# Kernel optimization log

Measured on AMD Instinct MI355X. Metric: run time of the kernel, lower is better.

## Reference

```python
import jax, jax.numpy as jnp
import numpy as np

MAX_CONTEXT = 100
NUM_HEADS = 4
GRU_GROUPS = 4


def _layernorm(x, g, b, eps=1e-5):
    m = jnp.mean(x, axis=-1, keepdims=True)
    v = jnp.mean((x - m) ** 2, axis=-1, keepdims=True)
    return (x - m) / jnp.sqrt(v + eps) * g + b


def _grouped_gru(x, wih, whh, bih, bhh, G):
    # x: [N, T, C]; shared GRU params run on each channel group (PyTorch gate order r,z,n)
    N, T, C = x.shape
    D = C // G
    xg = x.reshape(N, T, G, D)
    xp = jnp.einsum('ntgd,ed->ntge', xg, wih) + bih  # e = 3D, precomputed input projections
    xp = jnp.moveaxis(xp, 1, 0)  # [T, N, G, 3D]

    def step(h, xt):
        gh = jnp.einsum('ngd,ed->nge', h, whh) + bhh
        xr, xz, xn = jnp.split(xt, 3, axis=-1)
        hr, hz, hn = jnp.split(gh, 3, axis=-1)
        r = jax.nn.sigmoid(xr + hr)
        z = jax.nn.sigmoid(xz + hz)
        n = jnp.tanh(xn + r * hn)
        h = (1.0 - z) * n + z * h
        return h, h

    h0 = jnp.zeros((N, G, D), x.dtype)
    _, hs = jax.lax.scan(step, h0, xp)  # hs: [T, N, G, D]
    return jnp.moveaxis(hs, 0, 1).reshape(N, T, C)


def _mha(x, wqkv, bqkv, wo, bo, H, max_ctx):
    # batch_first self-attention with causal + truncated-window additive mask
    N, T, C = x.shape
    Dh = C // H
    qkv = x @ wqkv.T + bqkv
    q, k, v = jnp.split(qkv, 3, axis=-1)
    q = q.reshape(N, T, H, Dh)
    k = k.reshape(N, T, H, Dh)
    v = v.reshape(N, T, H, Dh)
    scale = 1.0 / np.sqrt(Dh).astype(np.float32)
    scores = jnp.einsum('nqhd,nkhd->nhqk', q, k) * scale
    i = jnp.arange(T)
    diff = i[:, None] - i[None, :]
    allowed = (diff >= 0) & (diff <= max_ctx)
    scores = jnp.where(allowed, scores, -jnp.inf)
    attn = jax.nn.softmax(scores, axis=-1)
    out = jnp.einsum('nhqk,nkhd->nqhd', attn, v).reshape(N, T, C)
    return out @ wo.T + bo


def setup_inputs() -> dict:
    key = jax.random.key(0)
    ks = jax.random.split(key, 5)
    B, C, T, F = 2, 128, 512, 64
    D = C // GRU_GROUPS
    s = 0.1
    return {
        'x': jax.random.normal(ks[0], (B, C, T, F), jnp.float32),
        'ln1_g': jnp.ones((C,), jnp.float32),
        'ln1_b': jnp.zeros((C,), jnp.float32),
        'gru_wih': jax.random.normal(ks[1], (3 * D, D), jnp.float32) * s,
        'gru_whh': jax.random.normal(ks[2], (3 * D, D), jnp.float32) * s,
        'gru_bih': jnp.zeros((3 * D,), jnp.float32),
        'gru_bhh': jnp.zeros((3 * D,), jnp.float32),
        'ln2_g': jnp.ones((C,), jnp.float32),
        'ln2_b': jnp.zeros((C,), jnp.float32),
        'in_proj_w': jax.random.normal(ks[3], (3 * C, C), jnp.float32) * s,
        'in_proj_b': jnp.zeros((3 * C,), jnp.float32),
        'out_proj_w': jax.random.normal(ks[4], (C, C), jnp.float32) * s,
        'out_proj_b': jnp.zeros((C,), jnp.float32),
    }


def reference(x, ln1_g, ln1_b, gru_wih, gru_whh, gru_bih, gru_bhh, ln2_g, ln2_b, in_proj_w, in_proj_b, out_proj_w, out_proj_b):
    B, C, T, F = x.shape
    # [B, C, T, F] -> [B*F, T, C]: each freq bin is an independent time sequence
    seq = jnp.transpose(x, (0, 3, 2, 1)).reshape(B * F, T, C)
    seq = seq + _grouped_gru(_layernorm(seq, ln1_g, ln1_b), gru_wih, gru_whh, gru_bih, gru_bhh, GRU_GROUPS)
    seq = seq + _mha(_layernorm(seq, ln2_g, ln2_b), in_proj_w, in_proj_b, out_proj_w, out_proj_b, NUM_HEADS, MAX_CONTEXT)
    return jnp.transpose(seq.reshape(B, F, T, C), (0, 3, 2, 1))
```

## Files before the change

### kernel.cpp

```cpp
#include <hip/hip_runtime.h>
#include <hip/hip_bf16.h>
#include <math.h>


typedef __attribute__((ext_vector_type(8))) short short8;
typedef __attribute__((ext_vector_type(4))) float f32x4;
typedef __attribute__((ext_vector_type(2))) float f32x2;

__device__ __forceinline__ float bflo(unsigned int u) { return __uint_as_float(u << 16); }
__device__ __forceinline__ float bfhi(unsigned int u) { return __uint_as_float(u & 0xffff0000u); }
__device__ __forceinline__ float bf2f(unsigned short u) { return __uint_as_float(((unsigned int)u) << 16); }
__device__ __forceinline__ unsigned short f2bf(float f) {
  __hip_bfloat16 h = __float2bfloat16(f);
  return *reinterpret_cast<unsigned short*>(&h);
}

typedef __attribute__((address_space(1))) const unsigned int uint_g;
typedef __attribute__((address_space(3))) unsigned int uint_l;
__device__ __forceinline__ void glds16(const void* g, void* l) {
  __builtin_amdgcn_global_load_lds((uint_g*)g, (uint_l*)l, 16, 0, 0);
}

__global__ void cvt_all_kernel(const float* __restrict__ a, unsigned short* __restrict__ da,
                               const float* __restrict__ b, unsigned short* __restrict__ db,
                               const float* __restrict__ c, unsigned short* __restrict__ dc) {
  int i = blockIdx.x * 256 + threadIdx.x;
  if (i < 3072) da[i] = f2bf(a[i]);
  else if (i < 3072 + 49152) db[i - 3072] = f2bf(b[i - 3072]);
  else if (i < 3072 + 49152 + 16384) dc[i - 52224] = f2bf(c[i - 52224]);
}

__global__ __launch_bounds__(256) void transpose_in_ln_kernel(const float* __restrict__ x,
                                                              float* __restrict__ seq,
                                                              const float* __restrict__ gam,
                                                              const float* __restrict__ bet,
                                                              unsigned short* __restrict__ out) {
  __shared__ float tile[128 * 65];
  int b = blockIdx.x >> 9;
  int t = blockIdx.x & 511;
  for (int i = threadIdx.x; i < 128 * 64; i += 256) {
    int c = i >> 6, f = i & 63;
    tile[c * 65 + f] = x[(((size_t)(b * 128 + c)) * 512 + t) * 64 + f];
  }
  __syncthreads();
  for (int i = threadIdx.x; i < 64 * 128; i += 256) {
    int f = i >> 7, c = i & 127;
    seq[(((size_t)(b * 64 + f)) * 512 + t) * 128 + c] = tile[c * 65 + f];
  }

  const int f = threadIdx.x >> 2, q = threadIdx.x & 3;
  float s = 0.f, ss = 0.f;
  #pragma unroll
  for (int u = 0; u < 32; ++u) {
    float v = tile[(q * 32 + u) * 65 + f];
    s += v; ss += v * v;
  }
  s += __shfl_xor(s, 1); s += __shfl_xor(s, 2);
  ss += __shfl_xor(ss, 1); ss += __shfl_xor(ss, 2);
  float mean = s * (1.f / 128.f);
  float var = ss * (1.f / 128.f) - mean * mean;
  float rs = rsqrtf(var + 1e-5f);

  unsigned int* orow = (unsigned int*)(out + (((size_t)(b * 64 + f)) * 512 + t) * 128);
  #pragma unroll
  for (int u = 0; u < 8; ++u) {
    int c0 = q * 32 + u * 4;
    float4 gg = ((const float4*)gam)[c0 >> 2];
    float4 bb = ((const float4*)bet)[c0 >> 2];
    float v0 = tile[(c0 + 0) * 65 + f], v1 = tile[(c0 + 1) * 65 + f];
    float v2 = tile[(c0 + 2) * 65 + f], v3 = tile[(c0 + 3) * 65 + f];
    float o0 = (v0 - mean) * rs * gg.x + bb.x;
    float o1 = (v1 - mean) * rs * gg.y + bb.y;
    float o2 = (v2 - mean) * rs * gg.z + bb.z;
    float o3 = (v3 - mean) * rs * gg.w + bb.w;
    orow[(c0 >> 1) + 0] = ((unsigned int)f2bf(o1) << 16) | (unsigned int)f2bf(o0);
    orow[(c0 >> 1) + 1] = ((unsigned int)f2bf(o3) << 16) | (unsigned int)f2bf(o2);
  }
}

__global__ __launch_bounds__(256) void transpose_out_kernel(const float* __restrict__ seq, float* __restrict__ out) {
  __shared__ float tile[128 * 65];
  int b = blockIdx.x >> 9;
  int t = blockIdx.x & 511;
  for (int i = threadIdx.x; i < 64 * 128; i += 256) {
    int f = i >> 7, c = i & 127;
    tile[c * 65 + f] = seq[(((size_t)(b * 64 + f)) * 512 + t) * 128 + c];
  }
  __syncthreads();
  for (int i = threadIdx.x; i < 128 * 64; i += 256) {
    int c = i >> 6, f = i & 63;
    out[(((size_t)(b * 128 + c)) * 512 + t) * 64 + f] = tile[c * 65 + f];
  }
}

__global__ __launch_bounds__(256) void ln_kernel(const float* __restrict__ in, const float* __restrict__ g,
                                                 const float* __restrict__ b, unsigned short* __restrict__ out) {
  int row = blockIdx.x * 4 + (threadIdx.x >> 6);
  int lane = threadIdx.x & 63;
  float2 v = ((const float2*)(in + (size_t)row * 128))[lane];
  float s = v.x + v.y, ss = v.x * v.x + v.y * v.y;
  #pragma unroll
  for (int off = 32; off > 0; off >>= 1) {
    s += __shfl_xor(s, off);
    ss += __shfl_xor(ss, off);
  }
  float mean = s * (1.f / 128.f);
  float var = ss * (1.f / 128.f) - mean * mean;
  float rs = rsqrtf(var + 1e-5f);
  float2 gg = ((const float2*)g)[lane];
  float2 bb = ((const float2*)b)[lane];
  float o0 = (v.x - mean) * rs * gg.x + bb.x;
  float o1 = (v.y - mean) * rs * gg.y + bb.y;
  unsigned int packed = ((unsigned int)f2bf(o1) << 16) | (unsigned int)f2bf(o0);
  ((unsigned int*)(out + (size_t)row * 128))[lane] = packed;
}

template <int K, int MODE>
__global__ __launch_bounds__(256) void gemm_mfma(const unsigned short* __restrict__ A,
                                                 const unsigned short* __restrict__ W,
                                                 const float* __restrict__ bias,
                                                 unsigned short* __restrict__ outB,
                                                 float* __restrict__ outF, int Ncols) {
  const int tid = threadIdx.x;
  const int wave = tid >> 6, lane = tid & 63;
  const int wy = wave >> 1, wx = wave & 1;
  const int lr = lane & 15, lq = lane >> 4;
  const int m0 = blockIdx.x * 128 + wy * 64;
  const int n0 = blockIdx.y * 128 + wx * 64;

  f32x4 acc[4][4];
  #pragma unroll
  for (int i = 0; i < 4; ++i)
    #pragma unroll
    for (int j = 0; j < 4; ++j) acc[i][j] = f32x4{0.f, 0.f, 0.f, 0.f};

  const short8 zfrag = short8{0, 0, 0, 0, 0, 0, 0, 0};

  #pragma unroll
  for (int kk = 0; kk < K; kk += 32) {
    short8 af[4], bfq[4];
    #pragma unroll
    for (int i = 0; i < 4; ++i)
      af[i] = *(const short8*)(A + (size_t)(m0 + i * 16 + lr) * K + kk + lq * 8);
    #pragma unroll
    for (int j = 0; j < 4; ++j) {
      int wr = n0 + j * 16 + lr;
      bfq[j] = (wr < Ncols) ? *(const short8*)(W + (size_t)wr * K + kk + lq * 8) : zfrag;
    }
    #pragma unroll
    for (int i = 0; i < 4; ++i)
      #pragma unroll
      for (int j = 0; j < 4; ++j)
        acc[i][j] = __builtin_amdgcn_mfma_f32_16x16x32_bf16(af[i], bfq[j], acc[i][j], 0, 0, 0);
  }

  #pragma unroll
  for (int j = 0; j < 4; ++j) {
    int col = n0 + j * 16 + lr;
    if (col < Ncols) {
      float bb = bias[col];
      #pragma unroll
      for (int i = 0; i < 4; ++i) {
        #pragma unroll
        for (int r = 0; r < 4; ++r) {
          int row = m0 + i * 16 + lq * 4 + r;
          float v = acc[i][j][r] + bb;
          if (MODE == 0)
            outB[(size_t)row * Ncols + col] = f2bf(v);
          else
            outF[(size_t)row * 128 + col] += v;
        }
      }
    }
  }
}

__global__ __launch_bounds__(64, 1) void gru_kernel(const unsigned short* __restrict__ xp,
                                                    const float* __restrict__ whh,
                                                    const float* __restrict__ bhh,
                                                    float* __restrict__ seq) {
  const int l = threadIdx.x;
  const int half = l >> 5, d = l & 31;
  const int blk = blockIdx.x;
  const int chain = blk * 2 + half;
  const int n = chain >> 2;
  const int g0 = (blk * 2) & 3;

  const float LOG2E = 1.4426950408889634f;
  const float T2LOG2E = 2.8853900817779268f;

  __shared__ __align__(16) unsigned char stage[2][6144];
  __shared__ __align__(16) float h_lds[2][64];
  h_lds[0][l] = 0.f;

  f32x2 wr2[16], wz2[16], wn2[16];
  #pragma unroll
  for (int u = 0; u < 16; ++u) {
    float2 a = *(const float2*)(whh + (size_t)d * 32 + u * 2);
    float2 b = *(const float2*)(whh + (size_t)(32 + d) * 32 + u * 2);
    float2 c = *(const float2*)(whh + (size_t)(64 + d) * 32 + u * 2);
    wr2[u] = f32x2{a.x * LOG2E, a.y * LOG2E};
    wz2[u] = f32x2{b.x * LOG2E, b.y * LOG2E};
    wn2[u] = f32x2{c.x * T2LOG2E, c.y * T2LOG2E};
  }
  #pragma unroll
  for (int u = 0; u < 16; ++u)
    asm volatile("" : "+v"(wr2[u]), "+v"(wz2[u]), "+v"(wn2[u]));

  float br = bhh[d] * LOG2E, bz = bhh[32 + d] * LOG2E, bn = bhh[64 + d] * T2LOG2E;
  asm volatile("" : "+v"(br), "+v"(bz), "+v"(bn));

  const char* xg = (const char*)xp;
  const size_t cb0 = ((size_t)n * 2048 + g0) * 192;
  const size_t cb1 = ((size_t)n * 2048 + g0 + 1) * 192;
  const int fa = l * 16;
  const int oxa = (fa / 192) * 768 + (fa % 192);
  const int fb = 1024 + l * 16;
  const int oxb = (fb / 192) * 768 + (fb % 192);
  const char* px0a = xg + cb0 + oxa;
  const char* px0b = xg + cb0 + oxb;
  const char* px1a = xg + cb1 + oxa;
  const char* px1b = xg + cb1 + oxb;
  const int osa = (l >> 4) * 512 + (l & 15) * 16;
  const size_t sqb0 = ((size_t)n * 512 * 128 + (size_t)g0 * 32) * 4;
  const char* psa = (const char*)seq + sqb0 + osa;
  const char* psb = psa + 2048;

  float* sb = seq + (size_t)n * 512 * 128 + g0 * 32 + l;

  glds16(px0a, stage[0] + 0);
  glds16(px0b, stage[0] + 1024);
  glds16(px1a, stage[0] + 2048);
  glds16(px1b, stage[0] + 3072);
  glds16(psa,  stage[0] + 4096);
  glds16(psb,  stage[0] + 5120);

  float hprev = 0.f;

  for (int c = 0; c < 64; ++c) {
    const int cur = c & 1;
    if (c < 63) {
      const size_t xo = (size_t)(c + 1) * 6144;
      const size_t so = (size_t)(c + 1) * 4096;
      unsigned char* nb = stage[cur ^ 1];
      glds16(px0a + xo, nb + 0);
      glds16(px0b + xo, nb + 1024);
      glds16(px1a + xo, nb + 2048);
      glds16(px1b + xo, nb + 3072);
      glds16(psa + so,  nb + 4096);
      glds16(psb + so,  nb + 5120);
    }
    __builtin_amdgcn_sched_barrier(0);
    if (c == 0)       asm volatile("s_waitcnt vmcnt(6)" ::: "memory");
    else if (c == 63) asm volatile("s_waitcnt vmcnt(8)" ::: "memory");
    else              asm volatile("s_waitcnt vmcnt(14)" ::: "memory");
    __builtin_amdgcn_sched_barrier(0);

    const unsigned char* scur = stage[cur];
    #pragma unroll
    for (int p = 0; p < 8; ++p) {
      const int t = c * 8 + p;

      const f32x4* hsrc = (const f32x4*)&h_lds[p & 1][half * 32];
      f32x2 ar0 = f32x2{br, 0.f}, ar1 = f32x2{0.f, 0.f};
      f32x2 az0 = f32x2{bz, 0.f}, az1 = f32x2{0.f, 0.f};
      f32x2 an0 = f32x2{bn, 0.f}, an1 = f32x2{0.f, 0.f};
      #pragma unroll
      for (int u = 0; u < 8; ++u) {
        f32x4 h4 = hsrc[u];
        f32x2 hlo = f32x2{h4.x, h4.y};
        f32x2 hhi = f32x2{h4.z, h4.w};
        ar0 += wr2[2 * u] * hlo; ar1 += wr2[2 * u + 1] * hhi;
        az0 += wz2[2 * u] * hlo; az1 += wz2[2 * u + 1] * hhi;
        an0 += wn2[2 * u] * hlo; an1 += wn2[2 * u + 1] * hhi;
      }
      f32x2 arv = ar0 + ar1, azv = az0 + az1, anv = an0 + an1;
      float accr = arv.x + arv.y;
      float accz = azv.x + azv.y;
      float accn = anv.x + anv.y;

      const unsigned short* xrow = (const unsigned short*)(scur + half * 2048 + p * 192);
      float xr = bf2f(xrow[d]) * LOG2E;
      float xz = bf2f(xrow[32 + d]) * LOG2E;
      float xn2 = bf2f(xrow[64 + d]) * T2LOG2E;
      float sv0 = *(const float*)(scur + 4096 + p * 256 + (l << 2));

      float r = __builtin_amdgcn_rcpf(1.f + __builtin_amdgcn_exp2f(-(xr + accr)));
      float z = __builtin_amdgcn_rcpf(1.f + __builtin_amdgcn_exp2f(-(xz + accz)));
      float e2 = __builtin_amdgcn_exp2f(xn2 + r * accn);
      float nn = 1.f - 2.f * __builtin_amdgcn_rcpf(e2 + 1.f);
      float hnew = z * (hprev - nn) + nn;
      hprev = hnew;

      h_lds[(p + 1) & 1][l] = hnew;
      sb[(size_t)t * 128] = sv0 + hnew;
    }
  }
}

__global__ __launch_bounds__(256) void attn_kernel(const unsigned short* __restrict__ qkv,
                                                   unsigned short* __restrict__ outp) {
  const int qbase = blockIdx.x * 64;
  const int h = blockIdx.y;
  const int n = blockIdx.z;
  const int tid = threadIdx.x;
  const int w = tid >> 6, lane = tid & 63;
  const int lr = lane & 15, lq = lane >> 4;
  const int ws0 = max(0, qbase - 100);

  const int KROWS = 192;
  const int VPITCH = 200;
  const int PPITCH = 40;

  __shared__ unsigned short KL[192 * 32];
  __shared__ unsigned short VT[32 * 200];
  __shared__ unsigned short PL[4][16 * 40];
  __shared__ float LL[64];

  const char* qkvb = (const char*)qkv;
  const size_t rowb = ((size_t)(n * 512 + ws0)) * 768;

  const int wq0 = qbase + w * 16;
  short8 qfrag = *(const short8*)(qkvb + ((size_t)(n * 512 + wq0 + lr)) * 768 + h * 64 + lq * 16);

  #pragma unroll
  for (int it = 0; it < 3; ++it) {
    int c = w * 192 + it * 64 + lane;
    const char* src = qkvb + rowb + (size_t)(c >> 2) * 768 + 256 + h * 64 + (size_t)(c & 3) * 16;
    glds16(src, (char*)KL + w * 3072 + it * 1024);
  }

  if (tid < KROWS) {
    const unsigned int* vsrc = (const unsigned int*)(qkvb + rowb + (size_t)tid * 768 + 512 + h * 64);
    #pragma unroll
    for (int u = 0; u < 16; ++u) {
      unsigned int vv = vsrc[u];
      VT[(2 * u) * VPITCH + tid] = (unsigned short)(vv & 0xffff);
      VT[(2 * u + 1) * VPITCH + tid] = (unsigned short)(vv >> 16);
    }
  }
  __syncthreads();

  const float SCL2 = 0.17677669529663687f * 1.4426950408889634f;
  const int lo = max(0, wq0 - 100) - ws0;
  const int hi = wq0 + 15 - ws0;
  const int kc0 = lo >> 5, kc1 = hi >> 5;

  f32x4 oacc0 = f32x4{0.f, 0.f, 0.f, 0.f};
  f32x4 oacc1 = f32x4{0.f, 0.f, 0.f, 0.f};
  float lsum[4] = {0.f, 0.f, 0.f, 0.f};
  unsigned short* plw = PL[w];

  for (int kc = kc0; kc <= kc1; ++kc) {
    #pragma unroll
    for (int sub = 0; sub < 2; ++sub) {
      const int kt = kc * 2 + sub;
      short8 kfrag = *(const short8*)(KL + (kt * 16 + lr) * 32 + lq * 8);
      f32x4 s4 = __builtin_amdgcn_mfma_f32_16x16x32_bf16(qfrag, kfrag,
                                                         f32x4{0.f, 0.f, 0.f, 0.f}, 0, 0, 0);
      const int tk = ws0 + kt * 16 + lr;
      #pragma unroll
      for (int r = 0; r < 4; ++r) {
        const int tq = wq0 + lq * 4 + r;
        bool ok = (tk <= tq) && (tk + 100 >= tq);
        float p = ok ? __builtin_amdgcn_exp2f(s4[r] * SCL2) : 0.f;
        lsum[r] += p;
        plw[(lq * 4 + r) * PPITCH + sub * 16 + lr] = f2bf(p);
      }
    }
    short8 pfrag = *(const short8*)(plw + lr * PPITCH + lq * 8);
    short8 vf0 = *(const short8*)(VT + lr * VPITCH + kc * 32 + lq * 8);
    short8 vf1 = *(const short8*)(VT + (16 + lr) * VPITCH + kc * 32 + lq * 8);
    oacc0 = __builtin_amdgcn_mfma_f32_16x16x32_bf16(vf0, pfrag, oacc0, 0, 0, 0);
    oacc1 = __builtin_amdgcn_mfma_f32_16x16x32_bf16(vf1, pfrag, oacc1, 0, 0, 0);
  }

  #pragma unroll
  for (int r = 0; r < 4; ++r) {
    float v = lsum[r];
    v += __shfl_xor(v, 1); v += __shfl_xor(v, 2);
    v += __shfl_xor(v, 4); v += __shfl_xor(v, 8);
    lsum[r] = v;
  }
  if (lr == 0) {
    #pragma unroll
    for (int r = 0; r < 4; ++r) LL[w * 16 + lq * 4 + r] = lsum[r];
  }
  float rl = __builtin_amdgcn_rcpf(LL[w * 16 + lr]);

  unsigned short* ob = outp + ((size_t)(n * 512 + wq0 + lr)) * 128 + h * 32 + lq * 4;
  {
    unsigned int w0 = ((unsigned int)f2bf(oacc0[1] * rl) << 16) | f2bf(oacc0[0] * rl);
    unsigned int w1 = ((unsigned int)f2bf(oacc0[3] * rl) << 16) | f2bf(oacc0[2] * rl);
    uint2 pk0; pk0.x = w0; pk0.y = w1;
    *(uint2*)ob = pk0;
    unsigned int w2 = ((unsigned int)f2bf(oacc1[1] * rl) << 16) | f2bf(oacc1[0] * rl);
    unsigned int w3 = ((unsigned int)f2bf(oacc1[3] * rl) << 16) | f2bf(oacc1[2] * rl);
    uint2 pk1; pk1.x = w2; pk1.y = w3;
    *(uint2*)(ob + 16) = pk1;
  }
}

extern "C" void kernel_launch(void* const* d_in, const int* in_sizes, int n_in,
                              void* d_out, int out_size, void* d_ws, size_t ws_size,
                              hipStream_t stream) {
  const float* x      = (const float*)d_in[0];
  const float* ln1_g  = (const float*)d_in[1];
  const float* ln1_b  = (const float*)d_in[2];
  const float* wih    = (const float*)d_in[3];
  const float* whh    = (const float*)d_in[4];
  const float* bih    = (const float*)d_in[5];
  const float* bhh    = (const float*)d_in[6];
  const float* ln2_g  = (const float*)d_in[7];
  const float* ln2_b  = (const float*)d_in[8];
  const float* inw    = (const float*)d_in[9];
  const float* inb    = (const float*)d_in[10];
  const float* outw   = (const float*)d_in[11];
  const float* outb   = (const float*)d_in[12];

  char* ws = (char*)d_ws;
  float*          seq   = (float*)ws;
  unsigned short* tmpb  = (unsigned short*)(ws + 33554432);
  unsigned short* big   = (unsigned short*)(ws + 50331648);
  unsigned short* wih_b = (unsigned short*)(ws + 100663296);
  unsigned short* inw_b = wih_b + 3072;
  unsigned short* outw_b = inw_b + 49152;

  cvt_all_kernel<<<269, 256, 0, stream>>>(wih, wih_b, inw, inw_b, outw, outw_b);

  transpose_in_ln_kernel<<<1024, 256, 0, stream>>>(x, seq, ln1_g, ln1_b, tmpb);

  gemm_mfma<32, 0><<<dim3(2048, 1), 256, 0, stream>>>(tmpb, wih_b, bih, big, nullptr, 96);

  gru_kernel<<<256, 64, 0, stream>>>(big, whh, bhh, seq);

  ln_kernel<<<16384, 256, 0, stream>>>(seq, ln2_g, ln2_b, tmpb);

  gemm_mfma<128, 0><<<dim3(512, 3), 256, 0, stream>>>(tmpb, inw_b, inb, big, nullptr, 384);

  attn_kernel<<<dim3(8, 4, 128), 256, 0, stream>>>(big, tmpb);

  gemm_mfma<128, 1><<<dim3(512, 1), 256, 0, stream>>>(tmpb, outw_b, outb, nullptr, seq, 128);

  transpose_out_kernel<<<1024, 256, 0, stream>>>(seq, (float*)d_out);
}
```

Baseline: 364.3 us.

## Fuse output projection into attention kernel and fold weight conversion into transpose

The attention kernel now loops over all four heads inside one block, stages the per-head bf16 outputs in shared memory, and applies the output projection with MFMA before adding the residual into seq. This removes the separate out-projection GEMM launch and the round trip of the attention output through global memory. Weight conversion to bf16 moves into the first transpose kernel, dropping one launch. The cost is fewer blocks in the attention grid (1024 instead of 4096), serialized head processing with extra syncs per block, and larger shared memory use, which may lower occupancy.

New measurement: 382.9 us. 1.05x slower.

```diff
diff --git a/kernel.cpp b/kernel.cpp
--- a/kernel.cpp
+++ b/kernel.cpp
@@ -21,20 +21,24 @@
   __builtin_amdgcn_global_load_lds((uint_g*)g, (uint_l*)l, 16, 0, 0);
 }
 
-__global__ void cvt_all_kernel(const float* __restrict__ a, unsigned short* __restrict__ da,
-                               const float* __restrict__ b, unsigned short* __restrict__ db,
-                               const float* __restrict__ c, unsigned short* __restrict__ dc) {
-  int i = blockIdx.x * 256 + threadIdx.x;
-  if (i < 3072) da[i] = f2bf(a[i]);
-  else if (i < 3072 + 49152) db[i - 3072] = f2bf(b[i - 3072]);
-  else if (i < 3072 + 49152 + 16384) dc[i - 52224] = f2bf(c[i - 52224]);
-}
-
 __global__ __launch_bounds__(256) void transpose_in_ln_kernel(const float* __restrict__ x,
                                                               float* __restrict__ seq,
                                                               const float* __restrict__ gam,
                                                               const float* __restrict__ bet,
-                                                              unsigned short* __restrict__ out) {
+                                                              unsigned short* __restrict__ out,
+                                                              const float* __restrict__ wih,
+                                                              unsigned short* __restrict__ wih_b,
+                                                              const float* __restrict__ inw,
+                                                              unsigned short* __restrict__ inw_b,
+                                                              const float* __restrict__ outw,
+                                                              unsigned short* __restrict__ outw_b) {
+  {
+    int g_ = blockIdx.x * 256 + threadIdx.x;
+    if (g_ < 3072) wih_b[g_] = f2bf(wih[g_]);
+    else if (g_ < 52224) inw_b[g_ - 3072] = f2bf(inw[g_ - 3072]);
+    else if (g_ < 68608) outw_b[g_ - 52224] = f2bf(outw[g_ - 52224]);
+  }
+
   __shared__ float tile[128 * 65];
   int b = blockIdx.x >> 9;
   int t = blockIdx.x & 511;
@@ -298,11 +302,12 @@
   }
 }
 
-__global__ __launch_bounds__(256) void attn_kernel(const unsigned short* __restrict__ qkv,
-                                                   unsigned short* __restrict__ outp) {
+__global__ __launch_bounds__(256) void attn_oproj_kernel(const unsigned short* __restrict__ qkv,
+                                                         const unsigned short* __restrict__ outw_b,
+                                                         const float* __restrict__ outb,
+                                                         float* __restrict__ seq) {
   const int qbase = blockIdx.x * 64;
-  const int h = blockIdx.y;
-  const int n = blockIdx.z;
+  const int n = blockIdx.y;
   const int tid = threadIdx.x;
   const int w = tid >> 6, lane = tid & 63;
   const int lr = lane & 15, lq = lane >> 4;
@@ -311,93 +316,122 @@
   const int KROWS = 192;
   const int VPITCH = 200;
   const int PPITCH = 40;
+  const int OPITCH = 132;
 
   __shared__ unsigned short KL[192 * 32];
   __shared__ unsigned short VT[32 * 200];
   __shared__ unsigned short PL[4][16 * 40];
   __shared__ float LL[64];
+  __shared__ unsigned short OT[64 * 132];
 
   const char* qkvb = (const char*)qkv;
   const size_t rowb = ((size_t)(n * 512 + ws0)) * 768;
-
   const int wq0 = qbase + w * 16;
-  short8 qfrag = *(const short8*)(qkvb + ((size_t)(n * 512 + wq0 + lr)) * 768 + h * 64 + lq * 16);
-
-  #pragma unroll
-  for (int it = 0; it < 3; ++it) {
-    int c = w * 192 + it * 64 + lane;
-    const char* src = qkvb + rowb + (size_t)(c >> 2) * 768 + 256 + h * 64 + (size_t)(c & 3) * 16;
-    glds16(src, (char*)KL + w * 3072 + it * 1024);
-  }
-
-  if (tid < KROWS) {
-    const unsigned int* vsrc = (const unsigned int*)(qkvb + rowb + (size_t)tid * 768 + 512 + h * 64);
-    #pragma unroll
-    for (int u = 0; u < 16; ++u) {
-      unsigned int vv = vsrc[u];
-      VT[(2 * u) * VPITCH + tid] = (unsigned short)(vv & 0xffff);
-      VT[(2 * u + 1) * VPITCH + tid] = (unsigned short)(vv >> 16);
-    }
-  }
-  __syncthreads();
 
   const float SCL2 = 0.17677669529663687f * 1.4426950408889634f;
   const int lo = max(0, wq0 - 100) - ws0;
   const int hi = wq0 + 15 - ws0;
   const int kc0 = lo >> 5, kc1 = hi >> 5;
-
-  f32x4 oacc0 = f32x4{0.f, 0.f, 0.f, 0.f};
-  f32x4 oacc1 = f32x4{0.f, 0.f, 0.f, 0.f};
-  float lsum[4] = {0.f, 0.f, 0.f, 0.f};
   unsigned short* plw = PL[w];
 
-  for (int kc = kc0; kc <= kc1; ++kc) {
-    #pragma unroll
-    for (int sub = 0; sub < 2; ++sub) {
-      const int kt = kc * 2 + sub;
-      short8 kfrag = *(const short8*)(KL + (kt * 16 + lr) * 32 + lq * 8);
-      f32x4 s4 = __builtin_amdgcn_mfma_f32_16x16x32_bf16(qfrag, kfrag,
-                                                         f32x4{0.f, 0.f, 0.f, 0.f}, 0, 0, 0);
-      const int tk = ws0 + kt * 16 + lr;
-      #pragma unroll
-      for (int r = 0; r < 4; ++r) {
-        const int tq = wq0 + lq * 4 + r;
-        bool ok = (tk <= tq) && (tk + 100 >= tq);
-        float p = ok ? __builtin_amdgcn_exp2f(s4[r] * SCL2) : 0.f;
-        lsum[r] += p;
-        plw[(lq * 4 + r) * PPITCH + sub * 16 + lr] = f2bf(p);
+  for (int h = 0; h < 4; ++h) {
+    if (h) __syncthreads();
+
+    #pragma unroll
+    for (int it = 0; it < 3; ++it) {
+      int c = w * 192 + it * 64 + lane;
+      const char* src = qkvb + rowb + (size_t)(c >> 2) * 768 + 256 + h * 64 + (size_t)(c & 3) * 16;
+      glds16(src, (char*)KL + w * 3072 + it * 1024);
+    }
+    if (tid < KROWS) {
+      const unsigned int* vsrc = (const unsigned int*)(qkvb + rowb + (size_t)tid * 768 + 512 + h * 64);
+      #pragma unroll
+      for (int u = 0; u < 16; ++u) {
+        unsigned int vv = vsrc[u];
+        VT[(2 * u) * VPITCH + tid] = (unsigned short)(vv & 0xffff);
+        VT[(2 * u + 1) * VPITCH + tid] = (unsigned short)(vv >> 16);
       }
     }
-    short8 pfrag = *(const short8*)(plw + lr * PPITCH + lq * 8);
-    short8 vf0 = *(const short8*)(VT + lr * VPITCH + kc * 32 + lq * 8);
-    short8 vf1 = *(const short8*)(VT + (16 + lr) * VPITCH + kc * 32 + lq * 8);
-    oacc0 = __builtin_amdgcn_mfma_f32_16x16x32_bf16(vf0, pfrag, oacc0, 0, 0, 0);
-    oacc1 = __builtin_amdgcn_mfma_f32_16x16x32_bf16(vf1, pfrag, oacc1, 0, 0, 0);
-  }
-
-  #pragma unroll
-  for (int r = 0; r < 4; ++r) {
-    float v = lsum[r];
-    v += __shfl_xor(v, 1); v += __shfl_xor(v, 2);
-    v += __shfl_xor(v, 4); v += __shfl_xor(v, 8);
-    lsum[r] = v;
-  }
-  if (lr == 0) {
-    #pragma unroll
-    for (int r = 0; r < 4; ++r) LL[w * 16 + lq * 4 + r] = lsum[r];
-  }
-  float rl = __builtin_amdgcn_rcpf(LL[w * 16 + lr]);
-
-  unsigned short* ob = outp + ((size_t)(n * 512 + wq0 + lr)) * 128 + h * 32 + lq * 4;
-  {
-    unsigned int w0 = ((unsigned int)f2bf(oacc0[1] * rl) << 16) | f2bf(oacc0[0] * rl);
-    unsigned int w1 = ((unsigned int)f2bf(oacc0[3] * rl) << 16) | f2bf(oacc0[2] * rl);
-    uint2 pk0; pk0.x = w0; pk0.y = w1;
-    *(uint2*)ob = pk0;
-    unsigned int w2 = ((unsigned int)f2bf(oacc1[1] * rl) << 16) | f2bf(oacc1[0] * rl);
-    unsigned int w3 = ((unsigned int)f2bf(oacc1[3] * rl) << 16) | f2bf(oacc1[2] * rl);
-    uint2 pk1; pk1.x = w2; pk1.y = w3;
-    *(uint2*)(ob + 16) = pk1;
+    short8 qfrag = *(const short8*)(qkvb + ((size_t)(n * 512 + wq0 + lr)) * 768 + h * 64 + lq * 16);
+    __syncthreads();
+
+    f32x4 oacc0 = f32x4{0.f, 0.f, 0.f, 0.f};
+    f32x4 oacc1 = f32x4{0.f, 0.f, 0.f, 0.f};
+    float lsum[4] = {0.f, 0.f, 0.f, 0.f};
+
+    for (int kc = kc0; kc <= kc1; ++kc) {
+      #pragma unroll
+      for (int sub = 0; sub < 2; ++sub) {
+        const int kt = kc * 2 + sub;
+        short8 kfrag = *(const short8*)(KL + (kt * 16 + lr) * 32 + lq * 8);
+        f32x4 s4 = __builtin_amdgcn_mfma_f32_16x16x32_bf16(qfrag, kfrag,
+                                                           f32x4{0.f, 0.f, 0.f, 0.f}, 0, 0, 0);
+        const int tk = ws0 + kt * 16 + lr;
+        #pragma unroll
+        for (int r = 0; r < 4; ++r) {
+          const int tq = wq0 + lq * 4 + r;
+          bool ok = (tk <= tq) && (tk + 100 >= tq);
+          float p = ok ? __builtin_amdgcn_exp2f(s4[r] * SCL2) : 0.f;
+          lsum[r] += p;
+          plw[(lq * 4 + r) * PPITCH + sub * 16 + lr] = f2bf(p);
+        }
+      }
+      short8 pfrag = *(const short8*)(plw + lr * PPITCH + lq * 8);
+      short8 vf0 = *(const short8*)(VT + lr * VPITCH + kc * 32 + lq * 8);
+      short8 vf1 = *(const short8*)(VT + (16 + lr) * VPITCH + kc * 32 + lq * 8);
+      oacc0 = __builtin_amdgcn_mfma_f32_16x16x32_bf16(vf0, pfrag, oacc0, 0, 0, 0);
+      oacc1 = __builtin_amdgcn_mfma_f32_16x16x32_bf16(vf1, pfrag, oacc1, 0, 0, 0);
+    }
+
+    #pragma unroll
+    for (int r = 0; r < 4; ++r) {
+      float v = lsum[r];
+      v += __shfl_xor(v, 1); v += __shfl_xor(v, 2);
+      v += __shfl_xor(v, 4); v += __shfl_xor(v, 8);
+      lsum[r] = v;
+    }
+    if (lr == 0) {
+      #pragma unroll
+      for (int r = 0; r < 4; ++r) LL[w * 16 + lq * 4 + r] = lsum[r];
+    }
+    float rl = __builtin_amdgcn_rcpf(LL[w * 16 + lr]);
+
+    {
+      unsigned short* orow = OT + (w * 16 + lr) * OPITCH + h * 32 + lq * 4;
+      uint2 pk0;
+      pk0.x = ((unsigned int)f2bf(oacc0[1] * rl) << 16) | f2bf(oacc0[0] * rl);
+      pk0.y = ((unsigned int)f2bf(oacc0[3] * rl) << 16) | f2bf(oacc0[2] * rl);
+      *(uint2*)orow = pk0;
+      uint2 pk1;
+      pk1.x = ((unsigned int)f2bf(oacc1[1] * rl) << 16) | f2bf(oacc1[0] * rl);
+      pk1.y = ((unsigned int)f2bf(oacc1[3] * rl) << 16) | f2bf(oacc1[2] * rl);
+      *(uint2*)(orow + 16) = pk1;
+    }
+  }
+
+  __syncthreads();
+
+  f32x4 acc[8];
+  #pragma unroll
+  for (int j = 0; j < 8; ++j) acc[j] = f32x4{0.f, 0.f, 0.f, 0.f};
+  #pragma unroll
+  for (int kk = 0; kk < 4; ++kk) {
+    short8 af = *(const short8*)(OT + (w * 16 + lr) * OPITCH + kk * 32 + lq * 8);
+    #pragma unroll
+    for (int j = 0; j < 8; ++j) {
+      short8 wf = *(const short8*)(outw_b + (size_t)(j * 16 + lr) * 128 + kk * 32 + lq * 8);
+      acc[j] = __builtin_amdgcn_mfma_f32_16x16x32_bf16(af, wf, acc[j], 0, 0, 0);
+    }
+  }
+  #pragma unroll
+  for (int j = 0; j < 8; ++j) {
+    int col = j * 16 + lr;
+    float bb = outb[col];
+    #pragma unroll
+    for (int r = 0; r < 4; ++r) {
+      size_t row = (size_t)n * 512 + qbase + w * 16 + lq * 4 + r;
+      seq[row * 128 + col] += acc[j][r] + bb;
+    }
   }
 }
 
@@ -426,9 +460,8 @@
   unsigned short* inw_b = wih_b + 3072;
   unsigned short* outw_b = inw_b + 49152;
 
-  cvt_all_kernel<<<269, 256, 0, stream>>>(wih, wih_b, inw, inw_b, outw, outw_b);
-
-  transpose_in_ln_kernel<<<1024, 256, 0, stream>>>(x, seq, ln1_g, ln1_b, tmpb);
+  transpose_in_ln_kernel<<<1024, 256, 0, stream>>>(x, seq, ln1_g, ln1_b, tmpb,
+                                                   wih, wih_b, inw, inw_b, outw, outw_b);
 
   gemm_mfma<32, 0><<<dim3(2048, 1), 256, 0, stream>>>(tmpb, wih_b, bih, big, nullptr, 96);
 
@@ -438,9 +471,7 @@
 
   gemm_mfma<128, 0><<<dim3(512, 3), 256, 0, stream>>>(tmpb, inw_b, inb, big, nullptr, 384);
 
-  attn_kernel<<<dim3(8, 4, 128), 256, 0, stream>>>(big, tmpb);
-
-  gemm_mfma<128, 1><<<dim3(512, 1), 256, 0, stream>>>(tmpb, outw_b, outb, nullptr, seq, 128);
+  attn_oproj_kernel<<<dim3(8, 128), 256, 0, stream>>>(big, outw_b, outb, seq);
 
   transpose_out_kernel<<<1024, 256, 0, stream>>>(seq, (float*)d_out);
 }
```
